# Kernel tuning notes

Measured on AMD Instinct MI355X. Metric: run time of the kernel, lower is better.

Reference implementation:

```python
import jax, jax.numpy as jnp
import numpy as np

D_MODEL = 512
HEADS = 8
D_FF = 1024
EPS = 1e-5


def layer_norm(x, gamma, beta):
    mu = jnp.mean(x, axis=-1, keepdims=True)
    var = jnp.mean(jnp.square(x - mu), axis=-1, keepdims=True)
    return (x - mu) * jax.lax.rsqrt(var + EPS) * gamma + beta


def mha(q, k, v, mask=None):
    # q,k,v: [B, S, D]; no input/output projections in the original module
    B, Sq, D = q.shape
    Sk = k.shape[1]
    dk = D // HEADS
    qh = q.reshape(B, Sq, HEADS, dk).transpose(0, 2, 1, 3)  # [B,H,Sq,dk]
    kh = k.reshape(B, Sk, HEADS, dk).transpose(0, 2, 1, 3)
    vh = v.reshape(B, Sk, HEADS, dk).transpose(0, 2, 1, 3)
    scores = jnp.einsum('bhqd,bhkd->bhqk', qh, kh) / np.sqrt(dk).astype(q.dtype)
    if mask is not None:
        scores = jnp.where(mask == 0, jnp.asarray(-1e9, scores.dtype), scores)
    attn = jax.nn.softmax(scores, axis=-1)  # dropout is identity in eval mode
    out = jnp.einsum('bhqk,bhkd->bhqd', attn, vh)
    return out.transpose(0, 2, 1, 3).reshape(B, Sq, D)


def setup_inputs() -> dict:
    key = jax.random.key(0)
    ks = jax.random.split(key, 8)
    B, S = 4, 2048
    x = jax.random.normal(ks[0], (B, S, D_MODEL), dtype=jnp.float32)
    encoder_output = jax.random.normal(ks[1], (B, S, D_MODEL), dtype=jnp.float32)
    mask = jax.random.randint(ks[2], (B, 1, S, S), 0, 2, dtype=jnp.int32)
    params = {
        'ln1_g': jnp.ones((D_MODEL,), jnp.float32), 'ln1_b': jnp.zeros((D_MODEL,), jnp.float32),
        'ln2_g': jnp.ones((D_MODEL,), jnp.float32), 'ln2_b': jnp.zeros((D_MODEL,), jnp.float32),
        'ln3_g': jnp.ones((D_MODEL,), jnp.float32), 'ln3_b': jnp.zeros((D_MODEL,), jnp.float32),
        'W1': jax.random.normal(ks[3], (D_MODEL, D_FF), jnp.float32) * (1.0 / np.sqrt(D_MODEL)),
        'b1': jnp.zeros((D_FF,), jnp.float32),
        'W2': jax.random.normal(ks[4], (D_FF, D_MODEL), jnp.float32) * (1.0 / np.sqrt(D_FF)),
        'b2': jnp.zeros((D_MODEL,), jnp.float32),
    }
    return {'x': x, 'encoder_output': encoder_output, 'mask': mask, **params}


def reference(x, encoder_output, mask, ln1_g, ln1_b, ln2_g, ln2_b, ln3_g, ln3_b, W1, b1, W2, b2):
    # pre-norm masked self-attention + residual (dropout = identity, eval mode)
    x1 = layer_norm(x, ln1_g, ln1_b)
    x = x + mha(x1, x1, x1, mask)
    # pre-norm cross-attention + residual
    x1 = layer_norm(x, ln2_g, ln2_b)
    x = x + mha(x1, encoder_output, encoder_output, None)
    # pre-norm FFN + residual
    x1 = layer_norm(x, ln3_g, ln3_b)
    h = jax.nn.relu(x1 @ W1 + b1)
    x = x + (h @ W2 + b2)
    return x
```

## Files before the change

kernel.cpp:

```cpp
#include <hip/hip_runtime.h>
#include <hip/hip_bf16.h>

#define D_MODEL 512
#define HEADS   8
#define DK      64
#define D_FF    1024
#define SEQ     2048
#define BATCH   4
#define NTOK    (BATCH*SEQ)
#define NELEM   (NTOK*D_MODEL)

#define QSCALE  0.18033688011112042f
#define MFIX    40.0f

typedef __attribute__((ext_vector_type(8))) short bf8_t;
typedef __attribute__((ext_vector_type(4))) float f4_t;

#define GLD16(gp, lp) __builtin_amdgcn_global_load_lds( \
    (const __attribute__((address_space(1))) void*)(gp), \
    (__attribute__((address_space(3))) void*)(lp), 16, 0, 0)

__device__ __forceinline__ float ldf(const void* p, size_t i, int f32) {
    return f32 ? ((const float*)p)[i] : __bfloat162float(((const __hip_bfloat16*)p)[i]);
}
__device__ __forceinline__ short f2bf(float f) {
    union { __hip_bfloat16 h; short s; } u; u.h = __float2bfloat16(f); return u.s;
}
__device__ __forceinline__ float bf2f(short s) {
    return __uint_as_float(((unsigned)(unsigned short)s) << 16);
}
__device__ __forceinline__ unsigned fbits(float f) { return __float_as_uint(f); }

__global__ void detect_k(const uint4* __restrict__ w, int* __restrict__ flags) {
    __shared__ int found;
    if (threadIdx.x == 0) found = 0;
    __syncthreads();
    int hit = 0;
    for (int i = threadIdx.x; i < 4096; i += 256) {
        uint4 u = w[i];
        if (((u.x & 0x7F80u) == 0x7F80u) || ((u.y & 0x7F80u) == 0x7F80u) ||
            ((u.z & 0x7F80u) == 0x7F80u) || ((u.w & 0x7F80u) == 0x7F80u)) hit = 1;
    }
    if (hit) atomicOr(&found, 1);
    __syncthreads();
    if (threadIdx.x == 0) flags[0] = found ? 1 : 0;
}

__device__ __forceinline__ void transpose_body(const void* src, __hip_bfloat16* dst,
                                               int K, int N, int bxi, int byi, int f32,
                                               __hip_bfloat16 (*t)[33]) {
    int bx = bxi * 32, by = byi * 32;
    int tx = threadIdx.x & 31, ty = threadIdx.x >> 5;
    #pragma unroll
    for (int j = 0; j < 32; j += 8)
        t[ty + j][tx] = __float2bfloat16(ldf(src, (size_t)(by + ty + j) * N + bx + tx, f32));
    __syncthreads();
    #pragma unroll
    for (int j = 0; j < 32; j += 8)
        dst[(size_t)(bx + ty + j) * K + by + tx] = t[tx][ty + j];
}

__global__ __launch_bounds__(256)
void prep_k(const void* __restrict__ enc, const int* __restrict__ mask,
            const void* __restrict__ W1, const void* __restrict__ W2,
            const int* __restrict__ flagp,
            __hip_bfloat16* __restrict__ bufE, unsigned* __restrict__ mb,
            __hip_bfloat16* __restrict__ W1T, __hip_bfloat16* __restrict__ W2T) {
    __shared__ __hip_bfloat16 t[32][33];
    int f32 = *flagp;
    int bid = blockIdx.x;
    if (bid < 16384) {
        int i = bid * 256 + threadIdx.x;
        bufE[i] = __float2bfloat16(ldf(enc, i, f32));
    } else if (bid < 18432) {
        int row  = (bid - 16384) * 4 + (threadIdx.x >> 6);
        int lane = threadIdx.x & 63;
        const int* mr = mask + (size_t)row * SEQ;
        for (int it = 0; it < SEQ/64; it++) {
            unsigned long long bal = __ballot(mr[it*64 + lane] != 0);
            if (lane == 0)  mb[(size_t)row*(SEQ/32) + it*2]     = (unsigned)bal;
            if (lane == 32) mb[(size_t)row*(SEQ/32) + it*2 + 1] = (unsigned)(bal >> 32);
        }
    } else if (bid < 18944) {
        int lb = bid - 18432;
        transpose_body(W1, W1T, D_MODEL, D_FF, lb & 31, lb >> 5, f32, t);
    } else {
        int lb = bid - 18944;
        transpose_body(W2, W2T, D_FF, D_MODEL, lb & 15, lb >> 4, f32, t);
    }
}

__global__ __launch_bounds__(256)
void ln_first_k(const void* __restrict__ x, const void* __restrict__ g,
                const void* __restrict__ b, const int* __restrict__ flagp,
                float* __restrict__ xout, __hip_bfloat16* __restrict__ y) {
    int f32  = *flagp;
    int row  = blockIdx.x * 4 + (threadIdx.x >> 6);
    int lane = threadIdx.x & 63;
    size_t base = (size_t)row * D_MODEL;
    float v[8];
    float s = 0.f;
    #pragma unroll
    for (int i = 0; i < 8; i++) { v[i] = ldf(x, base + lane + i*64, f32); s += v[i]; }
    #pragma unroll
    for (int off = 32; off; off >>= 1) s += __shfl_xor(s, off);
    float mu = s * (1.f / D_MODEL);
    float ss = 0.f;
    #pragma unroll
    for (int i = 0; i < 8; i++) { float d = v[i] - mu; ss += d * d; }
    #pragma unroll
    for (int off = 32; off; off >>= 1) ss += __shfl_xor(ss, off);
    float rstd = rsqrtf(ss * (1.f / D_MODEL) + 1e-5f);
    #pragma unroll
    for (int i = 0; i < 8; i++) {
        int c = lane + i*64;
        xout[base + c] = v[i];
        y[base + c] = __float2bfloat16((v[i] - mu) * rstd * ldf(g, c, f32) + ldf(b, c, f32));
    }
}

__global__ __launch_bounds__(256)
void layernorm_k(const float* __restrict__ x, const void* __restrict__ g,
                 const void* __restrict__ b, const int* __restrict__ flagp,
                 __hip_bfloat16* __restrict__ y) {
    int f32  = *flagp;
    int row  = blockIdx.x * 4 + (threadIdx.x >> 6);
    int lane = threadIdx.x & 63;
    const float* xr = x + (size_t)row * D_MODEL;
    float v[8];
    float s = 0.f;
    #pragma unroll
    for (int i = 0; i < 8; i++) { v[i] = xr[lane + i*64]; s += v[i]; }
    #pragma unroll
    for (int off = 32; off; off >>= 1) s += __shfl_xor(s, off);
    float mu = s * (1.f / D_MODEL);
    float ss = 0.f;
    #pragma unroll
    for (int i = 0; i < 8; i++) { float d = v[i] - mu; ss += d * d; }
    #pragma unroll
    for (int off = 32; off; off >>= 1) ss += __shfl_xor(ss, off);
    float rstd = rsqrtf(ss * (1.f / D_MODEL) + 1e-5f);
    __hip_bfloat16* yr = y + (size_t)row * D_MODEL;
    #pragma unroll
    for (int i = 0; i < 8; i++) {
        int c = lane + i*64;
        yr[c] = __float2bfloat16((v[i] - mu) * rstd * ldf(g, c, f32) + ldf(b, c, f32));
    }
}

__device__ __forceinline__ bf8_t prescale_q(bf8_t q) {
    bf8_t r;
    #pragma unroll
    for (int j = 0; j < 8; j++) r[j] = f2bf(bf2f(q[j]) * QSCALE);
    return r;
}

template<bool HAS_MASK>
__global__ __launch_bounds__(256, 2)
void attn_mfma_k(const __hip_bfloat16* __restrict__ Q, const __hip_bfloat16* __restrict__ K,
                 const __hip_bfloat16* __restrict__ V, const unsigned* __restrict__ mbits,
                 float* __restrict__ Xout) {
    int bid = blockIdx.x;
    int qt = bid & 15;
    int h  = (bid >> 4) & 7;
    int b  = bid >> 7;
    int q0 = qt * 128;
    int tid  = threadIdx.x;
    int w    = tid >> 6;
    int lane = tid & 63;
    int c    = lane & 15;
    int quad = lane >> 4;

    __shared__ __hip_bfloat16 Kt[2][64 * 64];
    __shared__ __hip_bfloat16 VT[2][64 * 64];
    __shared__ __hip_bfloat16 Pb[4][2][16 * 64];

    bf8_t qf[2][2];
    #pragma unroll
    for (int g = 0; g < 2; g++) {
        const __hip_bfloat16* qrp = Q + ((size_t)(b*SEQ + q0 + 32*w + 16*g + c)) * D_MODEL + h*DK;
        qf[g][0] = prescale_q(*(const bf8_t*)(qrp + quad*8));
        qf[g][1] = prescale_q(*(const bf8_t*)(qrp + 32 + quad*8));
    }

    int kpo[4][2], vpo[4][2];
    #pragma unroll
    for (int t = 0; t < 4; t++)
        #pragma unroll
        for (int kh = 0; kh < 2; kh++) {
            int row = 16*t + c;
            kpo[t][kh] = (row*64 + (((4*kh + quad) ^ (row & 7)) * 8)) * 2;
            vpo[t][kh] = (row*64 + (((4*kh + quad) ^ (row & 7) ^ ((row >> 3) & 7)) * 8)) * 2;
        }

    int key0 = (tid >> 3) * 2, d0 = (tid & 7) * 8;
    int vtwo[8];
    #pragma unroll
    for (int j = 0; j < 8; j++) {
        int dk = d0 + j;
        int ch = (key0 >> 3) ^ (dk & 7) ^ ((dk >> 3) & 7);
        vtwo[j] = dk*128 + ch*16 + (key0 & 7)*2;
    }

    int krow[2], kc8[2];
    #pragma unroll
    for (int i = 0; i < 2; i++) {
        int idx = i*256 + tid;
        krow[i] = idx >> 3;
        kc8[i]  = ((idx & 7) ^ (krow[i] & 7)) * 8;
    }

    char* pbw[2] = { (char*)&Pb[w][0][0], (char*)&Pb[w][1][0] };
    int pwoff[4], proff[2];
    #pragma unroll
    for (int nt = 0; nt < 4; nt++)
        pwoff[nt] = c*128 + (((2*nt + (quad >> 1)) ^ (c & 7)) * 16) + (quad & 1)*8;
    #pragma unroll
    for (int kh = 0; kh < 2; kh++)
        proff[kh] = c*128 + (((4*kh + quad) ^ (c & 7)) * 16);

    const unsigned* mrp[2] = {nullptr, nullptr};
    if (HAS_MASK) {
        mrp[0] = mbits + (size_t)(b*SEQ + q0 + 32*w + c) * (SEQ/32);
        mrp[1] = mrp[0] + (size_t)16 * (SEQ/32);
    }
    int qsh = quad * 4;

    short onev = (c == 0) ? (short)0x3F80 : (short)0;
    bf8_t ones = {onev, onev, onev, onev, onev, onev, onev, onev};

    f4_t o[2][4];
    #pragma unroll
    for (int g = 0; g < 2; g++)
        #pragma unroll
        for (int mt = 0; mt < 4; mt++) o[g][mt] = (f4_t){0.f,0.f,0.f,0.f};
    f4_t l_acc[2] = {(f4_t){0.f,0.f,0.f,0.f}, (f4_t){0.f,0.f,0.f,0.f}};

    const size_t kvbase = (size_t)b * SEQ * D_MODEL + (size_t)h * DK;

    for (int ph = 0; ph < SEQ/128; ph++) {
        int k0 = ph * 128;
        __syncthreads();
        #pragma unroll
        for (int t = 0; t < 2; t++) {
            const __hip_bfloat16* Kg = K + kvbase + (size_t)(k0 + t*64) * D_MODEL;
            GLD16(Kg + (size_t)krow[0]*D_MODEL + kc8[0], (char*)&Kt[t][0] + (w*64) * 16);
            GLD16(Kg + (size_t)krow[1]*D_MODEL + kc8[1], (char*)&Kt[t][0] + (256 + w*64) * 16);
        }
        #pragma unroll
        for (int t = 0; t < 2; t++) {
            const __hip_bfloat16* Vg = V + kvbase + (size_t)(k0 + t*64 + key0) * D_MODEL + d0;
            bf8_t v0 = *(const bf8_t*)Vg;
            bf8_t v1 = *(const bf8_t*)(Vg + D_MODEL);
            const unsigned* v0u = (const unsigned*)&v0;
            const unsigned* v1u = (const unsigned*)&v1;
            char* vb = (char*)&VT[t][0];
            #pragma unroll
            for (int dw = 0; dw < 4; dw++) {
                *(unsigned*)(vb + vtwo[2*dw])     = __builtin_amdgcn_perm(v1u[dw], v0u[dw], 0x05040100u);
                *(unsigned*)(vb + vtwo[2*dw + 1]) = __builtin_amdgcn_perm(v1u[dw], v0u[dw], 0x07060302u);
            }
        }
        __syncthreads();

        #pragma unroll
        for (int t = 0; t < 2; t++) {
            const char* ktb = (const char*)&Kt[t][0];
            const char* vtb = (const char*)&VT[t][0];

            f4_t s[2][4];
            #pragma unroll
            for (int nt = 0; nt < 4; nt++) { s[0][nt] = (f4_t){0.f,0.f,0.f,0.f}; s[1][nt] = (f4_t){0.f,0.f,0.f,0.f}; }
            #pragma unroll
            for (int nt = 0; nt < 4; nt++)
                #pragma unroll
                for (int kh = 0; kh < 2; kh++) {
                    bf8_t kf = *(const bf8_t*)(ktb + kpo[nt][kh]);
                    s[0][nt] = __builtin_amdgcn_mfma_f32_16x16x32_bf16(kf, qf[0][kh], s[0][nt], 0, 0, 0);
                    s[1][nt] = __builtin_amdgcn_mfma_f32_16x16x32_bf16(kf, qf[1][kh], s[1][nt], 0, 0, 0);
                }

            #pragma unroll
            for (int g = 0; g < 2; g++) {
                unsigned wq0 = 0xffffffffu, wq1 = 0xffffffffu;
                if (HAS_MASK) {
                    uint2 mw = *(const uint2*)(mrp[g] + ((k0 + t*64) >> 5));
                    wq0 = mw.x >> qsh; wq1 = mw.y >> qsh;
                }
                #pragma unroll
                for (int nt = 0; nt < 4; nt++) {
                    #pragma unroll
                    for (int r = 0; r < 4; r++) {
                        float p = exp2f(s[g][nt][r] - MFIX);
                        if (HAS_MASK) {
                            unsigned sel = (nt < 2) ? wq0 : wq1;
                            if (!((sel >> ((nt & 1)*16 + r)) & 1u)) p = 0.f;
                        }
                        s[g][nt][r] = p;
                    }
                    unsigned pk0 = __builtin_amdgcn_perm(fbits(s[g][nt][1]), fbits(s[g][nt][0]), 0x07060302u);
                    unsigned pk1 = __builtin_amdgcn_perm(fbits(s[g][nt][3]), fbits(s[g][nt][2]), 0x07060302u);
                    *(uint2*)(pbw[g] + pwoff[nt]) = make_uint2(pk0, pk1);
                }
            }

            #pragma unroll
            for (int kh = 0; kh < 2; kh++) {
                bf8_t pfA = *(const bf8_t*)(pbw[0] + proff[kh]);
                bf8_t pfB = *(const bf8_t*)(pbw[1] + proff[kh]);
                l_acc[0] = __builtin_amdgcn_mfma_f32_16x16x32_bf16(ones, pfA, l_acc[0], 0, 0, 0);
                l_acc[1] = __builtin_amdgcn_mfma_f32_16x16x32_bf16(ones, pfB, l_acc[1], 0, 0, 0);
                #pragma unroll
                for (int mt = 0; mt < 4; mt++) {
                    bf8_t vf = *(const bf8_t*)(vtb + vpo[mt][kh]);
                    o[0][mt] = __builtin_amdgcn_mfma_f32_16x16x32_bf16(vf, pfA, o[0][mt], 0, 0, 0);
                    o[1][mt] = __builtin_amdgcn_mfma_f32_16x16x32_bf16(vf, pfB, o[1][mt], 0, 0, 0);
                }
            }
        }
    }

    #pragma unroll
    for (int g = 0; g < 2; g++) {
        float lq = __shfl(l_acc[g][0], c);
        float il = 1.f / fmaxf(lq, 1e-35f);
        size_t rb = ((size_t)(b*SEQ + q0 + 32*w + 16*g + c)) * D_MODEL + h*DK;
        #pragma unroll
        for (int mt = 0; mt < 4; mt++)
            #pragma unroll
            for (int r = 0; r < 4; r++)
                Xout[rb + 16*mt + quad*4 + r] += o[g][mt][r] * il;
    }
}

__global__ __launch_bounds__(256, 2)
void gemm_relu_k(const __hip_bfloat16* __restrict__ A, const __hip_bfloat16* __restrict__ BT,
                 const void* __restrict__ bias, const int* __restrict__ flagp,
                 __hip_bfloat16* __restrict__ C, int Ksz, int Nsz) {
    int f32 = *flagp;
    __shared__ __hip_bfloat16 As[128 * 64];
    __shared__ __hip_bfloat16 Bs[128 * 64];
    int tid  = threadIdx.x;
    int w    = tid >> 6;
    int c    = tid & 15;
    int quad = (tid >> 4) & 3;
    int wy = w >> 1, wx = w & 1;
    int r0 = blockIdx.y * 128, c0 = blockIdx.x * 128;

    f4_t acc[4][4];
    #pragma unroll
    for (int i = 0; i < 4; i++)
        #pragma unroll
        for (int j = 0; j < 4; j++) acc[i][j] = (f4_t){0.f,0.f,0.f,0.f};

    for (int k0 = 0; k0 < Ksz; k0 += 64) {
        __syncthreads();
        #pragma unroll
        for (int i = 0; i < 4; i++) {
            int idx = i*256 + tid;
            int row = idx >> 3, c8 = idx & 7;
            GLD16(A  + (size_t)(r0 + row) * Ksz + k0 + ((c8 ^ (row & 7)) * 8),
                  (char*)As + (size_t)(i*256 + w*64) * 16);
            GLD16(BT + (size_t)(c0 + row) * Ksz + k0 + ((c8 ^ (row & 7)) * 8),
                  (char*)Bs + (size_t)(i*256 + w*64) * 16);
        }
        __syncthreads();

        #pragma unroll
        for (int kh = 0; kh < 2; kh++) {
            bf8_t af[4], bf[4];
            #pragma unroll
            for (int mt = 0; mt < 4; mt++) {
                int row = wy*64 + mt*16 + c;
                af[mt] = *(const bf8_t*)&As[row*64 + (((kh*4 + quad) ^ (row & 7)) * 8)];
            }
            #pragma unroll
            for (int nt = 0; nt < 4; nt++) {
                int row = wx*64 + nt*16 + c;
                bf[nt] = *(const bf8_t*)&Bs[row*64 + (((kh*4 + quad) ^ (row & 7)) * 8)];
            }
            #pragma unroll
            for (int mt = 0; mt < 4; mt++)
                #pragma unroll
                for (int nt = 0; nt < 4; nt++)
                    acc[mt][nt] = __builtin_amdgcn_mfma_f32_16x16x32_bf16(af[mt], bf[nt], acc[mt][nt], 0, 0, 0);
        }
    }

    #pragma unroll
    for (int mt = 0; mt < 4; mt++)
        #pragma unroll
        for (int nt = 0; nt < 4; nt++) {
            int col = c0 + wx*64 + nt*16 + c;
            float bv = ldf(bias, col, f32);
            #pragma unroll
            for (int r = 0; r < 4; r++) {
                int m = r0 + wy*64 + mt*16 + quad*4 + r;
                C[(size_t)m * Nsz + col] = __float2bfloat16(fmaxf(acc[mt][nt][r] + bv, 0.f));
            }
        }
}

__global__ __launch_bounds__(256, 2)
void gemm_out_k(const __hip_bfloat16* __restrict__ A, const __hip_bfloat16* __restrict__ BT,
                const void* __restrict__ bias, const float* __restrict__ resid,
                const int* __restrict__ flagp, void* __restrict__ out, int Ksz, int Nsz) {
    int f32 = *flagp;
    __shared__ __hip_bfloat16 As[128 * 64];
    __shared__ __hip_bfloat16 Bs[64 * 64];
    int tid  = threadIdx.x;
    int w    = tid >> 6;
    int c    = tid & 15;
    int quad = (tid >> 4) & 3;
    int r0 = blockIdx.y * 128, c0 = blockIdx.x * 64;

    f4_t acc[2][4];
    #pragma unroll
    for (int i = 0; i < 2; i++)
        #pragma unroll
        for (int j = 0; j < 4; j++) acc[i][j] = (f4_t){0.f,0.f,0.f,0.f};

    for (int k0 = 0; k0 < Ksz; k0 += 64) {
        __syncthreads();
        #pragma unroll
        for (int i = 0; i < 4; i++) {
            int idx = i*256 + tid;
            int row = idx >> 3, c8 = idx & 7;
            GLD16(A + (size_t)(r0 + row) * Ksz + k0 + ((c8 ^ (row & 7)) * 8),
                  (char*)As + (size_t)(i*256 + w*64) * 16);
        }
        #pragma unroll
        for (int i = 0; i < 2; i++) {
            int idx = i*256 + tid;
            int row = idx >> 3, c8 = idx & 7;
            GLD16(BT + (size_t)(c0 + row) * Ksz + k0 + ((c8 ^ (row & 7)) * 8),
                  (char*)Bs + (size_t)(i*256 + w*64) * 16);
        }
        __syncthreads();

        #pragma unroll
        for (int kh = 0; kh < 2; kh++) {
            bf8_t af[2], bf[4];
            #pragma unroll
            for (int mt = 0; mt < 2; mt++) {
                int row = w*32 + mt*16 + c;
                af[mt] = *(const bf8_t*)&As[row*64 + (((kh*4 + quad) ^ (row & 7)) * 8)];
            }
            #pragma unroll
            for (int nt = 0; nt < 4; nt++) {
                int row = nt*16 + c;
                bf[nt] = *(const bf8_t*)&Bs[row*64 + (((kh*4 + quad) ^ (row & 7)) * 8)];
            }
            #pragma unroll
            for (int mt = 0; mt < 2; mt++)
                #pragma unroll
                for (int nt = 0; nt < 4; nt++)
                    acc[mt][nt] = __builtin_amdgcn_mfma_f32_16x16x32_bf16(af[mt], bf[nt], acc[mt][nt], 0, 0, 0);
        }
    }

    #pragma unroll
    for (int mt = 0; mt < 2; mt++)
        #pragma unroll
        for (int nt = 0; nt < 4; nt++) {
            int col = c0 + nt*16 + c;
            float bv = ldf(bias, col, f32);
            #pragma unroll
            for (int r = 0; r < 4; r++) {
                int m = r0 + w*32 + mt*16 + quad*4 + r;
                float v = acc[mt][nt][r] + bv + resid[(size_t)m * Nsz + col];
                if (f32) ((float*)out)[(size_t)m * Nsz + col] = v;
                else     ((__hip_bfloat16*)out)[(size_t)m * Nsz + col] = __float2bfloat16(v);
            }
        }
}

extern "C" void kernel_launch(void* const* d_in, const int* in_sizes, int n_in,
                              void* d_out, int out_size, void* d_ws, size_t ws_size,
                              hipStream_t stream) {
    const void* x    = d_in[0];
    const void* enc  = d_in[1];
    const int*  mask = (const int*)d_in[2];
    const void* ln1g = d_in[3];
    const void* ln1b = d_in[4];
    const void* ln2g = d_in[5];
    const void* ln2b = d_in[6];
    const void* ln3g = d_in[7];
    const void* ln3b = d_in[8];
    const void* W1   = d_in[9];
    const void* b1   = d_in[10];
    const void* W2   = d_in[11];
    const void* b2   = d_in[12];

    char* ws = (char*)d_ws;
    float*          bufX  = (float*)ws;
    __hip_bfloat16* bufQ  = (__hip_bfloat16*)(ws + (16u<<20));
    __hip_bfloat16* bufE  = (__hip_bfloat16*)(ws + (24u<<20));
    __hip_bfloat16* bufH  = (__hip_bfloat16*)(ws + (32u<<20));
    __hip_bfloat16* W1T   = (__hip_bfloat16*)(ws + (48u<<20));
    __hip_bfloat16* W2T   = (__hip_bfloat16*)(ws + (49u<<20));
    unsigned*       mbits = (unsigned*)(ws + (50u<<20));
    int*            flags = (int*)(ws + (52u<<20));

    dim3 blk(256);
    detect_k<<<1, blk, 0, stream>>>((const uint4*)x, flags);
    prep_k<<<19456, blk, 0, stream>>>(enc, mask, W1, W2, flags, bufE, mbits, W1T, W2T);

    ln_first_k<<<NTOK/4, blk, 0, stream>>>(x, ln1g, ln1b, flags, bufX, bufQ);
    attn_mfma_k<true><<<BATCH*HEADS*(SEQ/128), blk, 0, stream>>>(bufQ, bufQ, bufQ, mbits, bufX);
    layernorm_k<<<NTOK/4, blk, 0, stream>>>(bufX, ln2g, ln2b, flags, bufQ);
    attn_mfma_k<false><<<BATCH*HEADS*(SEQ/128), blk, 0, stream>>>(bufQ, bufE, bufE, nullptr, bufX);
    layernorm_k<<<NTOK/4, blk, 0, stream>>>(bufX, ln3g, ln3b, flags, bufQ);
    gemm_relu_k<<<dim3(D_FF/128, NTOK/128), blk, 0, stream>>>(bufQ, W1T, b1, flags, bufH, D_MODEL, D_FF);
    gemm_out_k<<<dim3(D_MODEL/64, NTOK/128), blk, 0, stream>>>(bufH, W2T, b2, bufX, flags, d_out, D_FF, D_MODEL);
}
```

Before: 373.5 us.

## Fold first layernorm into prep, read K from global, retile FFN GEMMs

The first layernorm moves into the prep kernel as extra blocks, removing one launch. The attention kernel stops staging K in LDS and loads K fragments directly from global memory, and it processes 256 keys per phase with a 4-tile V transpose buffer. gemm_relu switches to a 128x64 tile and gemm_out to a 64x64 tile, both with launch bounds raised to 4 blocks per SM, which gives more blocks and higher occupancy but less reuse per tile. Loading K from global without LDS staging risks uncoalesced, latency-bound reads in the inner loop.

```diff
diff --git a/kernel.cpp b/kernel.cpp
--- a/kernel.cpp
+++ b/kernel.cpp
@@ -60,10 +60,40 @@
         dst[(size_t)(bx + ty + j) * K + by + tx] = t[tx][ty + j];
 }
 
+__device__ __forceinline__ void ln_body(const void* x, const void* g, const void* b,
+                                        int row, int f32, float* xout, __hip_bfloat16* y,
+                                        bool write_x) {
+    int lane = threadIdx.x & 63;
+    size_t base = (size_t)row * D_MODEL;
+    float v[8];
+    float s = 0.f;
+    #pragma unroll
+    for (int i = 0; i < 8; i++) { v[i] = (x == xout && !write_x) ? xout[base + lane + i*64]
+                                                                 : ldf(x, base + lane + i*64, f32); s += v[i]; }
+    #pragma unroll
+    for (int off = 32; off; off >>= 1) s += __shfl_xor(s, off);
+    float mu = s * (1.f / D_MODEL);
+    float ss = 0.f;
+    #pragma unroll
+    for (int i = 0; i < 8; i++) { float d = v[i] - mu; ss += d * d; }
+    #pragma unroll
+    for (int off = 32; off; off >>= 1) ss += __shfl_xor(ss, off);
+    float rstd = rsqrtf(ss * (1.f / D_MODEL) + 1e-5f);
+    #pragma unroll
+    for (int i = 0; i < 8; i++) {
+        int c = lane + i*64;
+        if (write_x) xout[base + c] = v[i];
+        y[base + c] = __float2bfloat16((v[i] - mu) * rstd * ldf(g, c, f32) + ldf(b, c, f32));
+    }
+}
+
 __global__ __launch_bounds__(256)
-void prep_k(const void* __restrict__ enc, const int* __restrict__ mask,
+void prep_k(const void* __restrict__ x, const void* __restrict__ enc,
+            const int* __restrict__ mask,
             const void* __restrict__ W1, const void* __restrict__ W2,
+            const void* __restrict__ ln1g, const void* __restrict__ ln1b,
             const int* __restrict__ flagp,
+            float* __restrict__ bufX, __hip_bfloat16* __restrict__ bufQ,
             __hip_bfloat16* __restrict__ bufE, unsigned* __restrict__ mb,
             __hip_bfloat16* __restrict__ W1T, __hip_bfloat16* __restrict__ W2T) {
     __shared__ __hip_bfloat16 t[32][33];
@@ -84,38 +114,12 @@
     } else if (bid < 18944) {
         int lb = bid - 18432;
         transpose_body(W1, W1T, D_MODEL, D_FF, lb & 31, lb >> 5, f32, t);
-    } else {
+    } else if (bid < 19456) {
         int lb = bid - 18944;
         transpose_body(W2, W2T, D_FF, D_MODEL, lb & 15, lb >> 4, f32, t);
-    }
-}
-
-__global__ __launch_bounds__(256)
-void ln_first_k(const void* __restrict__ x, const void* __restrict__ g,
-                const void* __restrict__ b, const int* __restrict__ flagp,
-                float* __restrict__ xout, __hip_bfloat16* __restrict__ y) {
-    int f32  = *flagp;
-    int row  = blockIdx.x * 4 + (threadIdx.x >> 6);
-    int lane = threadIdx.x & 63;
-    size_t base = (size_t)row * D_MODEL;
-    float v[8];
-    float s = 0.f;
-    #pragma unroll
-    for (int i = 0; i < 8; i++) { v[i] = ldf(x, base + lane + i*64, f32); s += v[i]; }
-    #pragma unroll
-    for (int off = 32; off; off >>= 1) s += __shfl_xor(s, off);
-    float mu = s * (1.f / D_MODEL);
-    float ss = 0.f;
-    #pragma unroll
-    for (int i = 0; i < 8; i++) { float d = v[i] - mu; ss += d * d; }
-    #pragma unroll
-    for (int off = 32; off; off >>= 1) ss += __shfl_xor(ss, off);
-    float rstd = rsqrtf(ss * (1.f / D_MODEL) + 1e-5f);
-    #pragma unroll
-    for (int i = 0; i < 8; i++) {
-        int c = lane + i*64;
-        xout[base + c] = v[i];
-        y[base + c] = __float2bfloat16((v[i] - mu) * rstd * ldf(g, c, f32) + ldf(b, c, f32));
+    } else {
+        int row = (bid - 19456) * 4 + (threadIdx.x >> 6);
+        ln_body(x, ln1g, ln1b, row, f32, bufX, bufQ, true);
     }
 }
 
@@ -125,27 +129,7 @@
                  __hip_bfloat16* __restrict__ y) {
     int f32  = *flagp;
     int row  = blockIdx.x * 4 + (threadIdx.x >> 6);
-    int lane = threadIdx.x & 63;
-    const float* xr = x + (size_t)row * D_MODEL;
-    float v[8];
-    float s = 0.f;
-    #pragma unroll
-    for (int i = 0; i < 8; i++) { v[i] = xr[lane + i*64]; s += v[i]; }
-    #pragma unroll
-    for (int off = 32; off; off >>= 1) s += __shfl_xor(s, off);
-    float mu = s * (1.f / D_MODEL);
-    float ss = 0.f;
-    #pragma unroll
-    for (int i = 0; i < 8; i++) { float d = v[i] - mu; ss += d * d; }
-    #pragma unroll
-    for (int off = 32; off; off >>= 1) ss += __shfl_xor(ss, off);
-    float rstd = rsqrtf(ss * (1.f / D_MODEL) + 1e-5f);
-    __hip_bfloat16* yr = y + (size_t)row * D_MODEL;
-    #pragma unroll
-    for (int i = 0; i < 8; i++) {
-        int c = lane + i*64;
-        yr[c] = __float2bfloat16((v[i] - mu) * rstd * ldf(g, c, f32) + ldf(b, c, f32));
-    }
+    ln_body(x, g, b, row, f32, (float*)x, y, false);
 }
 
 __device__ __forceinline__ bf8_t prescale_q(bf8_t q) {
@@ -171,8 +155,7 @@
     int c    = lane & 15;
     int quad = lane >> 4;
 
-    __shared__ __hip_bfloat16 Kt[2][64 * 64];
-    __shared__ __hip_bfloat16 VT[2][64 * 64];
+    __shared__ __hip_bfloat16 VT[4][64 * 64];
     __shared__ __hip_bfloat16 Pb[4][2][16 * 64];
 
     bf8_t qf[2][2];
@@ -183,13 +166,12 @@
         qf[g][1] = prescale_q(*(const bf8_t*)(qrp + 32 + quad*8));
     }
 
-    int kpo[4][2], vpo[4][2];
+    int vpo[4][2];
     #pragma unroll
     for (int t = 0; t < 4; t++)
         #pragma unroll
         for (int kh = 0; kh < 2; kh++) {
             int row = 16*t + c;
-            kpo[t][kh] = (row*64 + (((4*kh + quad) ^ (row & 7)) * 8)) * 2;
             vpo[t][kh] = (row*64 + (((4*kh + quad) ^ (row & 7) ^ ((row >> 3) & 7)) * 8)) * 2;
         }
 
@@ -202,14 +184,6 @@
         vtwo[j] = dk*128 + ch*16 + (key0 & 7)*2;
     }
 
-    int krow[2], kc8[2];
-    #pragma unroll
-    for (int i = 0; i < 2; i++) {
-        int idx = i*256 + tid;
-        krow[i] = idx >> 3;
-        kc8[i]  = ((idx & 7) ^ (krow[i] & 7)) * 8;
-    }
-
     char* pbw[2] = { (char*)&Pb[w][0][0], (char*)&Pb[w][1][0] };
     int pwoff[4], proff[2];
     #pragma unroll
@@ -238,22 +212,20 @@
 
     const size_t kvbase = (size_t)b * SEQ * D_MODEL + (size_t)h * DK;
 
-    for (int ph = 0; ph < SEQ/128; ph++) {
-        int k0 = ph * 128;
-        __syncthreads();
-        #pragma unroll
-        for (int t = 0; t < 2; t++) {
-            const __hip_bfloat16* Kg = K + kvbase + (size_t)(k0 + t*64) * D_MODEL;
-            GLD16(Kg + (size_t)krow[0]*D_MODEL + kc8[0], (char*)&Kt[t][0] + (w*64) * 16);
-            GLD16(Kg + (size_t)krow[1]*D_MODEL + kc8[1], (char*)&Kt[t][0] + (256 + w*64) * 16);
-        }
-        #pragma unroll
-        for (int t = 0; t < 2; t++) {
-            const __hip_bfloat16* Vg = V + kvbase + (size_t)(k0 + t*64 + key0) * D_MODEL + d0;
-            bf8_t v0 = *(const bf8_t*)Vg;
-            bf8_t v1 = *(const bf8_t*)(Vg + D_MODEL);
-            const unsigned* v0u = (const unsigned*)&v0;
-            const unsigned* v1u = (const unsigned*)&v1;
+    for (int ph = 0; ph < SEQ/256; ph++) {
+        int kb0 = ph * 256;
+        __syncthreads();
+        bf8_t v0[4], v1[4];
+        #pragma unroll
+        for (int t = 0; t < 4; t++) {
+            const __hip_bfloat16* Vg = V + kvbase + (size_t)(kb0 + t*64 + key0) * D_MODEL + d0;
+            v0[t] = *(const bf8_t*)Vg;
+            v1[t] = *(const bf8_t*)(Vg + D_MODEL);
+        }
+        #pragma unroll
+        for (int t = 0; t < 4; t++) {
+            const unsigned* v0u = (const unsigned*)&v0[t];
+            const unsigned* v1u = (const unsigned*)&v1[t];
             char* vb = (char*)&VT[t][0];
             #pragma unroll
             for (int dw = 0; dw < 4; dw++) {
@@ -264,27 +236,30 @@
         __syncthreads();
 
         #pragma unroll
-        for (int t = 0; t < 2; t++) {
-            const char* ktb = (const char*)&Kt[t][0];
+        for (int t = 0; t < 4; t++) {
+            int kb = kb0 + t*64;
+            const __hip_bfloat16* Kg = K + kvbase + (size_t)kb * D_MODEL;
             const char* vtb = (const char*)&VT[t][0];
 
             f4_t s[2][4];
             #pragma unroll
             for (int nt = 0; nt < 4; nt++) { s[0][nt] = (f4_t){0.f,0.f,0.f,0.f}; s[1][nt] = (f4_t){0.f,0.f,0.f,0.f}; }
             #pragma unroll
-            for (int nt = 0; nt < 4; nt++)
+            for (int nt = 0; nt < 4; nt++) {
+                const __hip_bfloat16* krow = Kg + (size_t)(16*nt + c) * D_MODEL + quad*8;
                 #pragma unroll
                 for (int kh = 0; kh < 2; kh++) {
-                    bf8_t kf = *(const bf8_t*)(ktb + kpo[nt][kh]);
+                    bf8_t kf = *(const bf8_t*)(krow + kh*32);
                     s[0][nt] = __builtin_amdgcn_mfma_f32_16x16x32_bf16(kf, qf[0][kh], s[0][nt], 0, 0, 0);
                     s[1][nt] = __builtin_amdgcn_mfma_f32_16x16x32_bf16(kf, qf[1][kh], s[1][nt], 0, 0, 0);
                 }
+            }
 
             #pragma unroll
             for (int g = 0; g < 2; g++) {
                 unsigned wq0 = 0xffffffffu, wq1 = 0xffffffffu;
                 if (HAS_MASK) {
-                    uint2 mw = *(const uint2*)(mrp[g] + ((k0 + t*64) >> 5));
+                    uint2 mw = *(const uint2*)(mrp[g] + (kb >> 5));
                     wq0 = mw.x >> qsh; wq1 = mw.y >> qsh;
                 }
                 #pragma unroll
@@ -333,78 +308,10 @@
     }
 }
 
-__global__ __launch_bounds__(256, 2)
+__global__ __launch_bounds__(256, 4)
 void gemm_relu_k(const __hip_bfloat16* __restrict__ A, const __hip_bfloat16* __restrict__ BT,
                  const void* __restrict__ bias, const int* __restrict__ flagp,
                  __hip_bfloat16* __restrict__ C, int Ksz, int Nsz) {
-    int f32 = *flagp;
-    __shared__ __hip_bfloat16 As[128 * 64];
-    __shared__ __hip_bfloat16 Bs[128 * 64];
-    int tid  = threadIdx.x;
-    int w    = tid >> 6;
-    int c    = tid & 15;
-    int quad = (tid >> 4) & 3;
-    int wy = w >> 1, wx = w & 1;
-    int r0 = blockIdx.y * 128, c0 = blockIdx.x * 128;
-
-    f4_t acc[4][4];
-    #pragma unroll
-    for (int i = 0; i < 4; i++)
-        #pragma unroll
-        for (int j = 0; j < 4; j++) acc[i][j] = (f4_t){0.f,0.f,0.f,0.f};
-
-    for (int k0 = 0; k0 < Ksz; k0 += 64) {
-        __syncthreads();
-        #pragma unroll
-        for (int i = 0; i < 4; i++) {
-            int idx = i*256 + tid;
-            int row = idx >> 3, c8 = idx & 7;
-            GLD16(A  + (size_t)(r0 + row) * Ksz + k0 + ((c8 ^ (row & 7)) * 8),
-                  (char*)As + (size_t)(i*256 + w*64) * 16);
-            GLD16(BT + (size_t)(c0 + row) * Ksz + k0 + ((c8 ^ (row & 7)) * 8),
-                  (char*)Bs + (size_t)(i*256 + w*64) * 16);
-        }
-        __syncthreads();
-
-        #pragma unroll
-        for (int kh = 0; kh < 2; kh++) {
-            bf8_t af[4], bf[4];
-            #pragma unroll
-            for (int mt = 0; mt < 4; mt++) {
-                int row = wy*64 + mt*16 + c;
-                af[mt] = *(const bf8_t*)&As[row*64 + (((kh*4 + quad) ^ (row & 7)) * 8)];
-            }
-            #pragma unroll
-            for (int nt = 0; nt < 4; nt++) {
-                int row = wx*64 + nt*16 + c;
-                bf[nt] = *(const bf8_t*)&Bs[row*64 + (((kh*4 + quad) ^ (row & 7)) * 8)];
-            }
-            #pragma unroll
-            for (int mt = 0; mt < 4; mt++)
-                #pragma unroll
-                for (int nt = 0; nt < 4; nt++)
-                    acc[mt][nt] = __builtin_amdgcn_mfma_f32_16x16x32_bf16(af[mt], bf[nt], acc[mt][nt], 0, 0, 0);
-        }
-    }
-
-    #pragma unroll
-    for (int mt = 0; mt < 4; mt++)
-        #pragma unroll
-        for (int nt = 0; nt < 4; nt++) {
-            int col = c0 + wx*64 + nt*16 + c;
-            float bv = ldf(bias, col, f32);
-            #pragma unroll
-            for (int r = 0; r < 4; r++) {
-                int m = r0 + wy*64 + mt*16 + quad*4 + r;
-                C[(size_t)m * Nsz + col] = __float2bfloat16(fmaxf(acc[mt][nt][r] + bv, 0.f));
-            }
-        }
-}
-
-__global__ __launch_bounds__(256, 2)
-void gemm_out_k(const __hip_bfloat16* __restrict__ A, const __hip_bfloat16* __restrict__ BT,
-                const void* __restrict__ bias, const float* __restrict__ resid,
-                const int* __restrict__ flagp, void* __restrict__ out, int Ksz, int Nsz) {
     int f32 = *flagp;
     __shared__ __hip_bfloat16 As[128 * 64];
     __shared__ __hip_bfloat16 Bs[64 * 64];
@@ -468,11 +375,66 @@
             #pragma unroll
             for (int r = 0; r < 4; r++) {
                 int m = r0 + w*32 + mt*16 + quad*4 + r;
-                float v = acc[mt][nt][r] + bv + resid[(size_t)m * Nsz + col];
-                if (f32) ((float*)out)[(size_t)m * Nsz + col] = v;
-                else     ((__hip_bfloat16*)out)[(size_t)m * Nsz + col] = __float2bfloat16(v);
-            }
-        }
+                C[(size_t)m * Nsz + col] = __float2bfloat16(fmaxf(acc[mt][nt][r] + bv, 0.f));
+            }
+        }
+}
+
+__global__ __launch_bounds__(256, 4)
+void gemm_out_k(const __hip_bfloat16* __restrict__ A, const __hip_bfloat16* __restrict__ BT,
+                const void* __restrict__ bias, const float* __restrict__ resid,
+                const int* __restrict__ flagp, void* __restrict__ out, int Ksz, int Nsz) {
+    int f32 = *flagp;
+    __shared__ __hip_bfloat16 As[64 * 64];
+    __shared__ __hip_bfloat16 Bs[64 * 64];
+    int tid  = threadIdx.x;
+    int w    = tid >> 6;
+    int c    = tid & 15;
+    int quad = (tid >> 4) & 3;
+    int r0 = blockIdx.y * 64, c0 = blockIdx.x * 64;
+
+    f4_t acc[4];
+    #pragma unroll
+    for (int j = 0; j < 4; j++) acc[j] = (f4_t){0.f,0.f,0.f,0.f};
+
+    for (int k0 = 0; k0 < Ksz; k0 += 64) {
+        __syncthreads();
+        #pragma unroll
+        for (int i = 0; i < 2; i++) {
+            int idx = i*256 + tid;
+            int row = idx >> 3, c8 = idx & 7;
+            GLD16(A + (size_t)(r0 + row) * Ksz + k0 + ((c8 ^ (row & 7)) * 8),
+                  (char*)As + (size_t)(i*256 + w*64) * 16);
+            GLD16(BT + (size_t)(c0 + row) * Ksz + k0 + ((c8 ^ (row & 7)) * 8),
+                  (char*)Bs + (size_t)(i*256 + w*64) * 16);
+        }
+        __syncthreads();
+
+        #pragma unroll
+        for (int kh = 0; kh < 2; kh++) {
+            int arow = w*16 + c;
+            bf8_t af = *(const bf8_t*)&As[arow*64 + (((kh*4 + quad) ^ (arow & 7)) * 8)];
+            #pragma unroll
+            for (int nt = 0; nt < 4; nt++) {
+                int row = nt*16 + c;
+                bf8_t bf = *(const bf8_t*)&Bs[row*64 + (((kh*4 + quad) ^ (row & 7)) * 8)];
+                acc[nt] = __builtin_amdgcn_mfma_f32_16x16x32_bf16(af, bf, acc[nt], 0, 0, 0);
+            }
+        }
+    }
+
+    #pragma unroll
+    for (int nt = 0; nt < 4; nt++) {
+        int col = c0 + nt*16 + c;
+        float bv = ldf(bias, col, f32);
+        #pragma unroll
+        for (int r = 0; r < 4; r++) {
+            int m = r0 + w*16 + quad*4 + r;
+            float v = acc[nt][r] + bv + resid[(size_t)m * Nsz + col];
+            if (f32) ((float*)out)[(size_t)m * Nsz + col] = v;
+            else     ((__hip_bfloat16*)out)[(size_t)m * Nsz + col] = __float2bfloat16(v);
+        }
+    }
 }
 
 extern "C" void kernel_launch(void* const* d_in, const int* in_sizes, int n_in,
@@ -504,13 +466,13 @@
 
     dim3 blk(256);
     detect_k<<<1, blk, 0, stream>>>((const uint4*)x, flags);
-    prep_k<<<19456, blk, 0, stream>>>(enc, mask, W1, W2, flags, bufE, mbits, W1T, W2T);
-
-    ln_first_k<<<NTOK/4, blk, 0, stream>>>(x, ln1g, ln1b, flags, bufX, bufQ);
+    prep_k<<<21504, blk, 0, stream>>>(x, enc, mask, W1, W2, ln1g, ln1b, flags,
+                                      bufX, bufQ, bufE, mbits, W1T, W2T);
+
     attn_mfma_k<true><<<BATCH*HEADS*(SEQ/128), blk, 0, stream>>>(bufQ, bufQ, bufQ, mbits, bufX);
     layernorm_k<<<NTOK/4, blk, 0, stream>>>(bufX, ln2g, ln2b, flags, bufQ);
     attn_mfma_k<false><<<BATCH*HEADS*(SEQ/128), blk, 0, stream>>>(bufQ, bufE, bufE, nullptr, bufX);
     layernorm_k<<<NTOK/4, blk, 0, stream>>>(bufX, ln3g, ln3b, flags, bufQ);
-    gemm_relu_k<<<dim3(D_FF/128, NTOK/128), blk, 0, stream>>>(bufQ, W1T, b1, flags, bufH, D_MODEL, D_FF);
-    gemm_out_k<<<dim3(D_MODEL/64, NTOK/128), blk, 0, stream>>>(bufH, W2T, b2, bufX, flags, d_out, D_FF, D_MODEL);
-}
+    gemm_relu_k<<<dim3(D_FF/64, NTOK/128), blk, 0, stream>>>(bufQ, W1T, b1, flags, bufH, D_MODEL, D_FF);
+    gemm_out_k<<<dim3(D_MODEL/64, NTOK/64), blk, 0, stream>>>(bufH, W2T, b2, bufX, flags, d_out, D_FF, D_MODEL);
+}
```

Measured after the change: 418.0 us. 11.9% more time.
